# Performance work log

Hardware: AMD Instinct MI355X
Metric: run time of the kernel (lower is better)

The kernel has to match this reference:

```python
import jax, jax.numpy as jnp
import numpy as np

NUM_HEADS = 32  # head_dim = input_dim // num_heads = 32 == C (forced by matmul contraction)


def setup_inputs() -> dict:
    key = jax.random.key(0)
    ks = jax.random.split(key, 8)
    B, C, D3, H1 = 16, 32, 1, 32
    input_dim = 1024  # == C**2, forced by the final view(B, C, H1, W1)
    s = 0.02
    x1 = jax.random.normal(ks[0], (B, C, D3, H1, input_dim), jnp.float32)
    x2 = jax.random.normal(ks[1], (B, C, D3, H1, input_dim), jnp.float32)
    Wq = jax.random.normal(ks[2], (input_dim, input_dim), jnp.float32) * s
    bq = jax.random.normal(ks[3], (input_dim,), jnp.float32) * s
    Wk = jax.random.normal(ks[4], (input_dim, input_dim), jnp.float32) * s
    bk = jax.random.normal(ks[5], (input_dim,), jnp.float32) * s
    Wv = jax.random.normal(ks[6], (input_dim, input_dim), jnp.float32) * s
    bv = jax.random.normal(ks[7], (input_dim,), jnp.float32) * s
    return {"x1": x1, "x2": x2, "Wq": Wq, "bq": bq, "Wk": Wk, "bk": bk, "Wv": Wv, "bv": bv}


def reference(x1, x2, Wq, bq, Wk, bk, Wv, bv):
    B, C, _, H1, W1 = x1.shape  # W1 == input_dim (Linear acts on last dim)
    nh = NUM_HEADS
    hd = W1 // nh
    # Linear projections on the last axis (torch Linear: x @ W.T + b)
    q = (x1 @ Wq.T + bq).reshape(B, C, nh, hd, -1).transpose(0, 2, 4, 3, 1)  # (B, nh, L1, hd, C)
    k = (x2 @ Wk.T + bk).reshape(B, C, nh, hd, -1)                            # (B, C, nh, hd, L2)
    v = (x2 @ Wv.T + bv).reshape(B, C, nh, hd, -1)                            # (B, C, nh, hd, L2)
    # Broadcasted batched matmul: contracts q's trailing C axis with k's hd axis (C == hd).
    energy = jnp.matmul(q, k)                      # (B, C, L1, hd, L2)
    attention = jax.nn.softmax(energy, axis=-1)    # softmax over L2
    # Contracts v's L2 axis with attention's hd axis (L2 == hd).
    out = jnp.matmul(v, attention)                 # (B, C, L1, hd, L2)
    out = out.transpose(0, 2, 4, 3, 1).reshape(B, C, H1, W1)
    return out
```

## Files before the change

### kernel.cpp

```cpp
#include <hip/hip_runtime.h>
#include <cstdint>

typedef __bf16 bf16x8 __attribute__((ext_vector_type(8)));
typedef float f32x4 __attribute__((ext_vector_type(4)));
typedef unsigned short us8 __attribute__((ext_vector_type(8)));

__device__ __forceinline__ unsigned short f2bf(float f) {
  union { float f; uint32_t u; } c; c.f = f;
  uint32_t u = c.u + 0x7FFFu + ((c.u >> 16) & 1u);
  return (unsigned short)(u >> 16);
}

__global__ __launch_bounds__(256) void cvt5(
    const float* __restrict__ x1, const float* __restrict__ x2,
    const float* __restrict__ Wq, const float* __restrict__ Wk, const float* __restrict__ Wv,
    unsigned short* __restrict__ xb1, unsigned short* __restrict__ xb2,
    unsigned short* __restrict__ wb) {
  int z = blockIdx.y;
  const float* src; unsigned short* dst; int n4;
  if (z == 0)      { src = x1; dst = xb1;            n4 = 16777216 / 4; }
  else if (z == 1) { src = x2; dst = xb2;            n4 = 16777216 / 4; }
  else if (z == 2) { src = Wq; dst = wb;             n4 = 1048576 / 4; }
  else if (z == 3) { src = Wk; dst = wb + 1048576;   n4 = 1048576 / 4; }
  else             { src = Wv; dst = wb + 2*1048576; n4 = 1048576 / 4; }
  for (int i = blockIdx.x * 256 + threadIdx.x; i < n4; i += gridDim.x * 256) {
    float4 v = ((const float4*)src)[i];
    ushort4 o;
    o.x = f2bf(v.x); o.y = f2bf(v.y); o.z = f2bf(v.z); o.w = f2bf(v.w);
    ((ushort4*)dst)[i] = o;
  }
}

__global__ __launch_bounds__(256) void gemm_qkv(
    const unsigned short* __restrict__ xb1, const unsigned short* __restrict__ xb2,
    const unsigned short* __restrict__ wb,
    const float* __restrict__ bq, const float* __restrict__ bk, const float* __restrict__ bv,
    unsigned short* __restrict__ qkv) {
  __shared__ __attribute__((aligned(16))) unsigned short lA[128 * 32];
  __shared__ __attribute__((aligned(16))) unsigned short lB[128 * 32];
  const int id = blockIdx.x;
  const int xcd = id & 7;
  const int j = id >> 3;
  const int nb = j & 7;
  const int g = j >> 3;
  const int z = g >> 4;
  const int mb = (g & 15) * 8 + xcd;
  const unsigned short* A = (z == 0) ? xb1 : xb2;
  const unsigned short* W = wb + z * 1048576;
  const float* bias = (z == 0) ? bq : (z == 1 ? bk : bv);
  unsigned short* C = qkv + z * 16777216;
  const int n0 = nb * 128;
  const int m0 = mb * 128;
  const int lane = threadIdx.x & 63;
  const int wv = threadIdx.x >> 6;
  const int wm = wv >> 1, wn = wv & 1;
  const int mr = lane & 15, quad = lane >> 4;

  f32x4 acc[4][4];
#pragma unroll
  for (int i = 0; i < 4; ++i)
#pragma unroll
    for (int jj = 0; jj < 4; ++jj) acc[i][jj] = (f32x4){0.f, 0.f, 0.f, 0.f};

  for (int k0 = 0; k0 < 1024; k0 += 32) {
#pragma unroll
    for (int c4 = 0; c4 < 4; ++c4) {
      int c = wv * 4 + c4;
      int isB = c >> 3;
      int cc = c & 7;
      int row = cc * 16 + (lane >> 2);
      const unsigned short* src = isB ? (W + (n0 + row) * 1024 + k0)
                                      : (A + (m0 + row) * 1024 + k0);
      const char* gp = (const char*)src + (lane & 3) * 16;
      char* ldst = (char*)(isB ? lB : lA) + cc * 1024;
      __builtin_amdgcn_global_load_lds((const __attribute__((address_space(1))) void*)gp,
                                       (__attribute__((address_space(3))) void*)ldst,
                                       16, 0, 0);
    }
    __syncthreads();
    bf16x8 af[4], bfr[4];
#pragma unroll
    for (int i = 0; i < 4; ++i)
      af[i] = *(const bf16x8*)(lA + (wm * 64 + i * 16 + mr) * 32 + quad * 8);
#pragma unroll
    for (int jj = 0; jj < 4; ++jj)
      bfr[jj] = *(const bf16x8*)(lB + (wn * 64 + jj * 16 + mr) * 32 + quad * 8);
#pragma unroll
    for (int i = 0; i < 4; ++i)
#pragma unroll
      for (int jj = 0; jj < 4; ++jj)
        acc[i][jj] = __builtin_amdgcn_mfma_f32_16x16x32_bf16(af[i], bfr[jj], acc[i][jj], 0, 0, 0);
    __syncthreads();
  }
#pragma unroll
  for (int jj = 0; jj < 4; ++jj) {
    int col = n0 + wn * 64 + jj * 16 + mr;
    float bb = bias[col];
#pragma unroll
    for (int i = 0; i < 4; ++i) {
      int rbase = m0 + wm * 64 + i * 16 + quad * 4;
#pragma unroll
      for (int r = 0; r < 4; ++r)
        C[(rbase + r) * 1024 + col] = f2bf(acc[i][jj][r] + bb);
    }
  }
}

__global__ __launch_bounds__(256) void attn(const unsigned short* __restrict__ qkv,
                                            float* __restrict__ obuf) {
  const unsigned short* qbuf = qkv;
  const unsigned short* kbuf = qkv + 16777216;
  const unsigned short* vbuf = qkv + 2 * 16777216;
  __shared__ __attribute__((aligned(16))) unsigned short qs[8192];
  __shared__ __attribute__((aligned(16))) unsigned short ks[4][1024];
  __shared__ __attribute__((aligned(16))) unsigned short vs[4][1024];
  __shared__ __attribute__((aligned(16))) unsigned short ats[4][1024];
  const int id = blockIdx.x;
  const int xcd = id & 7;
  const int pos = id >> 3;
  const int y0 = (pos & 3) * 8;
  const int bx = (pos >> 2) * 8 + xcd;
  const int b = bx >> 5;
  const int x = bx & 31;
  const int lane = threadIdx.x & 63;
  const int wv = threadIdx.x >> 6;
  const int mr = lane & 15, quad = lane >> 4;

#pragma unroll
  for (int it = 0; it < 4; ++it) {
    int c = threadIdx.x + 256 * it;
    int t = c >> 5, m = c & 31;
    const uint4* src = (const uint4*)(qbuf + ((b * 1024 + t * 32 + x) * 1024 + m * 32 + y0));
    ((uint4*)qs)[c] = *src;
  }
  __syncthreads();

  for (int s = 0; s < 2; ++s) {
    int y = y0 + wv * 2 + s;
    int dy = wv * 2 + s;
    const unsigned short* krow = kbuf + ((b * 32 + x) * 32 + y) * 1024;
    const unsigned short* vrow = vbuf + ((b * 32 + x) * 32 + y) * 1024;
    ((uint4*)ks[wv])[lane] = ((const uint4*)krow)[lane];
    ((uint4*)ks[wv])[64 + lane] = ((const uint4*)krow)[64 + lane];
    ((uint4*)vs[wv])[lane] = ((const uint4*)vrow)[lane];
    ((uint4*)vs[wv])[64 + lane] = ((const uint4*)vrow)[64 + lane];

    bf16x8 qa[2], kb[2];
#pragma unroll
    for (int mt = 0; mt < 2; ++mt) {
      us8 tmp;
#pragma unroll
      for (int jj = 0; jj < 8; ++jj)
        tmp[jj] = qs[((quad * 8 + jj) * 32 + mt * 16 + mr) * 8 + dy];
      qa[mt] = __builtin_bit_cast(bf16x8, tmp);
    }
#pragma unroll
    for (int lt = 0; lt < 2; ++lt) {
      us8 tmp;
#pragma unroll
      for (int jj = 0; jj < 8; ++jj)
        tmp[jj] = ks[wv][(quad * 8 + jj) * 32 + lt * 16 + mr];
      kb[lt] = __builtin_bit_cast(bf16x8, tmp);
    }
    f32x4 e[2][2];
#pragma unroll
    for (int mt = 0; mt < 2; ++mt)
#pragma unroll
      for (int lt = 0; lt < 2; ++lt) {
        f32x4 zz = (f32x4){0.f, 0.f, 0.f, 0.f};
        e[mt][lt] = __builtin_amdgcn_mfma_f32_16x16x32_bf16(qa[mt], kb[lt], zz, 0, 0, 0);
      }

#pragma unroll
    for (int mt = 0; mt < 2; ++mt)
#pragma unroll
      for (int r = 0; r < 4; ++r) {
        float v0 = e[mt][0][r], v1 = e[mt][1][r];
        float mx = fmaxf(v0, v1);
#pragma unroll
        for (int off = 1; off < 16; off <<= 1) mx = fmaxf(mx, __shfl_xor(mx, off));
        float p0 = __expf(v0 - mx), p1 = __expf(v1 - mx);
        float sm = p0 + p1;
#pragma unroll
        for (int off = 1; off < 16; off <<= 1) sm += __shfl_xor(sm, off);
        float inv = 1.0f / sm;
        p0 *= inv; p1 *= inv;
        int trow = mt * 16 + quad * 4 + r;
        ats[wv][trow * 32 + mr] = f2bf(p0);
        ats[wv][trow * 32 + 16 + mr] = f2bf(p1);
      }

    bf16x8 va[2], pb[2];
#pragma unroll
    for (int i = 0; i < 2; ++i)
      va[i] = *(const bf16x8*)(&vs[wv][(i * 16 + mr) * 32 + quad * 8]);
#pragma unroll
    for (int lt = 0; lt < 2; ++lt) {
      us8 tmp;
#pragma unroll
      for (int jj = 0; jj < 8; ++jj)
        tmp[jj] = ats[wv][(quad * 8 + jj) * 32 + lt * 16 + mr];
      pb[lt] = __builtin_bit_cast(bf16x8, tmp);
    }
    f32x4 o[2][2];
#pragma unroll
    for (int i = 0; i < 2; ++i)
#pragma unroll
      for (int lt = 0; lt < 2; ++lt) {
        f32x4 zz = (f32x4){0.f, 0.f, 0.f, 0.f};
        o[i][lt] = __builtin_amdgcn_mfma_f32_16x16x32_bf16(va[i], pb[lt], zz, 0, 0, 0);
      }

    float* orow = obuf + ((b * 32 + x) * 32 + y) * 1024;
#pragma unroll
    for (int i = 0; i < 2; ++i)
#pragma unroll
      for (int lt = 0; lt < 2; ++lt)
#pragma unroll
        for (int r = 0; r < 4; ++r)
          orow[(i * 16 + quad * 4 + r) * 32 + lt * 16 + mr] = o[i][lt][r];
  }
}

__global__ __launch_bounds__(256) void transpose2(const float* __restrict__ obuf,
                                                  float* __restrict__ out) {
  __shared__ float t[2][32][33];
  const int y = blockIdx.y, b = blockIdx.z;
  int l = threadIdx.x & 31;
  int g = threadIdx.x >> 5;
#pragma unroll
  for (int mi = 0; mi < 8; ++mi) {
    int m = blockIdx.x * 8 + mi;
    int buf = mi & 1;
    for (int xx = g; xx < 32; xx += 8)
      t[buf][xx][l] = obuf[((b * 32 + xx) * 32 + y) * 1024 + m * 32 + l];
    __syncthreads();
    for (int ll = g; ll < 32; ll += 8)
      out[((b * 32 + y) * 32 + ll) * 1024 + m * 32 + l] = t[buf][l][ll];
  }
}

extern "C" void kernel_launch(void* const* d_in, const int* in_sizes, int n_in,
                              void* d_out, int out_size, void* d_ws, size_t ws_size,
                              hipStream_t stream) {
  const float* x1 = (const float*)d_in[0];
  const float* x2 = (const float*)d_in[1];
  const float* Wq = (const float*)d_in[2];
  const float* bq = (const float*)d_in[3];
  const float* Wk = (const float*)d_in[4];
  const float* bk = (const float*)d_in[5];
  const float* Wv = (const float*)d_in[6];
  const float* bv = (const float*)d_in[7];
  float* out = (float*)d_out;

  char* ws = (char*)d_ws;
  unsigned short* xb1 = (unsigned short*)ws;
  unsigned short* xb2 = xb1 + 16777216;
  unsigned short* wb = xb2 + 16777216;
  unsigned short* qkv = wb + 3 * 1048576;
  float* obuf = (float*)ws;

  cvt5<<<dim3(2048, 5), 256, 0, stream>>>(x1, x2, Wq, Wk, Wv, xb1, xb2, wb);
  gemm_qkv<<<dim3(3072), 256, 0, stream>>>(xb1, xb2, wb, bq, bk, bv, qkv);
  attn<<<dim3(2048), 256, 0, stream>>>(qkv, obuf);
  transpose2<<<dim3(4, 32, 16), 256, 0, stream>>>(obuf, out);
}
```

Measured before the change: 360.5 us.

## Rewrite QKV GEMM as 256x256 double-buffered pipelined kernel with swizzled LDS

Replaces the 128x128, single-buffered QKV projection GEMM with a 256x256 tile, 512-thread kernel using BK=64. Global-to-LDS loads are double-buffered and interleaved with MFMA phases under barriers and setprio. The LDS layout uses an XOR swizzle to avoid bank conflicts. Block IDs are remapped per XCD for cache locality. The aim is to hide load latency and raise data reuse in the dominant GEMM, at the cost of 128KB of LDS per block, lower occupancy and a fragile hand-written waitcnt schedule.

Result: no change. 357.6 us (-0.8%).

```diff
diff --git a/kernel.cpp b/kernel.cpp
--- a/kernel.cpp
+++ b/kernel.cpp
@@ -31,77 +31,161 @@
   }
 }
 
-__global__ __launch_bounds__(256) void gemm_qkv(
+__device__ __forceinline__ void stage_half(const unsigned short* __restrict__ g,
+                                           unsigned short* l, int wv, int rl, int cg) {
+#pragma unroll
+  for (int ld = 0; ld < 2; ++ld) {
+    const int chunk = wv * 2 + ld;
+    const unsigned short* gp = g + (chunk * 8 + rl) * 1024 + cg * 8;
+    unsigned short* lp = l + chunk * 512;
+    __builtin_amdgcn_global_load_lds((const __attribute__((address_space(1))) void*)gp,
+                                     (__attribute__((address_space(3))) void*)lp,
+                                     16, 0, 0);
+  }
+}
+
+__global__ __launch_bounds__(512) void gemm_qkv(
     const unsigned short* __restrict__ xb1, const unsigned short* __restrict__ xb2,
     const unsigned short* __restrict__ wb,
     const float* __restrict__ bq, const float* __restrict__ bk, const float* __restrict__ bv,
     unsigned short* __restrict__ qkv) {
-  __shared__ __attribute__((aligned(16))) unsigned short lA[128 * 32];
-  __shared__ __attribute__((aligned(16))) unsigned short lB[128 * 32];
+  __shared__ __attribute__((aligned(16))) unsigned short sm[65536];
+  unsigned short* lA0 = sm;
+  unsigned short* lB0 = sm + 16384;
+  unsigned short* lA1 = sm + 32768;
+  unsigned short* lB1 = sm + 49152;
+
   const int id = blockIdx.x;
-  const int xcd = id & 7;
-  const int j = id >> 3;
-  const int nb = j & 7;
-  const int g = j >> 3;
-  const int z = g >> 4;
-  const int mb = (g & 15) * 8 + xcd;
-  const unsigned short* A = (z == 0) ? xb1 : xb2;
-  const unsigned short* W = wb + z * 1048576;
+  const int swz = (id & 7) * 96 + (id >> 3);
+  const int z = swz >> 8;
+  const int rem = swz & 255;
+  const int mb = rem >> 2;
+  const int nb = rem & 3;
+  const int m0 = mb * 256;
+  const int n0 = nb * 256;
+
+  const unsigned short* Ag = (z == 0) ? xb1 : xb2;
+  const unsigned short* Wg = wb + z * 1048576;
   const float* bias = (z == 0) ? bq : (z == 1 ? bk : bv);
   unsigned short* C = qkv + z * 16777216;
-  const int n0 = nb * 128;
-  const int m0 = mb * 128;
-  const int lane = threadIdx.x & 63;
-  const int wv = threadIdx.x >> 6;
-  const int wm = wv >> 1, wn = wv & 1;
-  const int mr = lane & 15, quad = lane >> 4;
-
-  f32x4 acc[4][4];
-#pragma unroll
-  for (int i = 0; i < 4; ++i)
-#pragma unroll
-    for (int jj = 0; jj < 4; ++jj) acc[i][jj] = (f32x4){0.f, 0.f, 0.f, 0.f};
-
-  for (int k0 = 0; k0 < 1024; k0 += 32) {
-#pragma unroll
-    for (int c4 = 0; c4 < 4; ++c4) {
-      int c = wv * 4 + c4;
-      int isB = c >> 3;
-      int cc = c & 7;
-      int row = cc * 16 + (lane >> 2);
-      const unsigned short* src = isB ? (W + (n0 + row) * 1024 + k0)
-                                      : (A + (m0 + row) * 1024 + k0);
-      const char* gp = (const char*)src + (lane & 3) * 16;
-      char* ldst = (char*)(isB ? lB : lA) + cc * 1024;
-      __builtin_amdgcn_global_load_lds((const __attribute__((address_space(1))) void*)gp,
-                                       (__attribute__((address_space(3))) void*)ldst,
-                                       16, 0, 0);
-    }
-    __syncthreads();
-    bf16x8 af[4], bfr[4];
+
+  const int tid = threadIdx.x;
+  const int lane = tid & 63;
+  const int wv = tid >> 6;
+  const int wm = wv >> 2;
+  const int wn = wv & 3;
+  const int mr = lane & 15;
+  const int quad = lane >> 4;
+
+  const int rl = lane >> 3;
+  const int cg = (lane & 7) ^ rl;
+
+  const int sg0 = ((quad) ^ (mr & 7)) * 8;
+  const int sg1 = ((4 + quad) ^ (mr & 7)) * 8;
+  const int arow = (wm * 128 + mr) * 64;
+  const int brow = (wn * 64 + mr) * 64;
+
+  f32x4 acc[8][4];
+#pragma unroll
+  for (int i = 0; i < 8; ++i)
+#pragma unroll
+    for (int j = 0; j < 4; ++j) acc[i][j] = (f32x4){0.f, 0.f, 0.f, 0.f};
+
+  bf16x8 af[4][2], bfr[4][2];
+
+  auto STA = [&](unsigned short* dst, int kt) {
+    const unsigned short* g = Ag + m0 * 1024 + kt * 64;
+    stage_half(g, dst, wv, rl, cg);
+    stage_half(g + 128 * 1024, dst + 8192, wv, rl, cg);
+  };
+  auto STB = [&](unsigned short* dst, int kt) {
+    const unsigned short* g = Wg + n0 * 1024 + kt * 64;
+    stage_half(g, dst, wv, rl, cg);
+    stage_half(g + 128 * 1024, dst + 8192, wv, rl, cg);
+  };
+  auto RDA = [&](const unsigned short* lA, int ib) {
+#pragma unroll
+    for (int i = 0; i < 4; ++i) {
+      af[i][0] = *(const bf16x8*)(lA + arow + (ib + i) * 1024 + sg0);
+      af[i][1] = *(const bf16x8*)(lA + arow + (ib + i) * 1024 + sg1);
+    }
+  };
+  auto RDB = [&](const unsigned short* lB, int jb) {
+#pragma unroll
+    for (int j = 0; j < 2; ++j) {
+      bfr[jb + j][0] = *(const bf16x8*)(lB + brow + (jb + j) * 1024 + sg0);
+      bfr[jb + j][1] = *(const bf16x8*)(lB + brow + (jb + j) * 1024 + sg1);
+    }
+  };
+  auto MF = [&](int ib, int jb) {
 #pragma unroll
     for (int i = 0; i < 4; ++i)
-      af[i] = *(const bf16x8*)(lA + (wm * 64 + i * 16 + mr) * 32 + quad * 8);
-#pragma unroll
-    for (int jj = 0; jj < 4; ++jj)
-      bfr[jj] = *(const bf16x8*)(lB + (wn * 64 + jj * 16 + mr) * 32 + quad * 8);
-#pragma unroll
-    for (int i = 0; i < 4; ++i)
-#pragma unroll
-      for (int jj = 0; jj < 4; ++jj)
-        acc[i][jj] = __builtin_amdgcn_mfma_f32_16x16x32_bf16(af[i], bfr[jj], acc[i][jj], 0, 0, 0);
-    __syncthreads();
-  }
-#pragma unroll
-  for (int jj = 0; jj < 4; ++jj) {
-    int col = n0 + wn * 64 + jj * 16 + mr;
-    float bb = bias[col];
-#pragma unroll
-    for (int i = 0; i < 4; ++i) {
-      int rbase = m0 + wm * 64 + i * 16 + quad * 4;
+#pragma unroll
+      for (int j = 0; j < 2; ++j)
+#pragma unroll
+        for (int h = 0; h < 2; ++h)
+          acc[ib + i][jb + j] = __builtin_amdgcn_mfma_f32_16x16x32_bf16(
+              af[i][h], bfr[jb + j][h], acc[ib + i][jb + j], 0, 0, 0);
+  };
+
+  STA(lA0, 0);
+  STB(lB0, 0);
+  STA(lA1, 1);
+  asm volatile("s_waitcnt vmcnt(4)" ::: "memory");
+  __builtin_amdgcn_s_barrier();
+
+#pragma unroll 1
+  for (int t = 0; t < 8; ++t) {
+    const bool lastt = (t == 7);
+    RDA(lA0, 0); RDB(lB0, 0);
+    STB(lB1, 2 * t + 1);
+    __builtin_amdgcn_s_barrier();
+    __builtin_amdgcn_s_setprio(1); MF(0, 0); __builtin_amdgcn_s_setprio(0);
+    __builtin_amdgcn_s_barrier();
+    RDB(lB0, 2);
+    __builtin_amdgcn_s_barrier();
+    __builtin_amdgcn_s_setprio(1); MF(0, 2); __builtin_amdgcn_s_setprio(0);
+    __builtin_amdgcn_s_barrier();
+    RDA(lA0, 4);
+    __builtin_amdgcn_s_barrier();
+    __builtin_amdgcn_s_setprio(1); MF(4, 0); __builtin_amdgcn_s_setprio(0);
+    __builtin_amdgcn_s_barrier();
+    if (!lastt) STA(lA0, 2 * t + 2);
+    __builtin_amdgcn_s_barrier();
+    __builtin_amdgcn_s_setprio(1); MF(4, 2); __builtin_amdgcn_s_setprio(0);
+    if (lastt) { asm volatile("s_waitcnt vmcnt(0)" ::: "memory"); }
+    else       { asm volatile("s_waitcnt vmcnt(4)" ::: "memory"); }
+    __builtin_amdgcn_s_barrier();
+    RDA(lA1, 0); RDB(lB1, 0);
+    if (!lastt) STB(lB0, 2 * t + 2);
+    __builtin_amdgcn_s_barrier();
+    __builtin_amdgcn_s_setprio(1); MF(0, 0); __builtin_amdgcn_s_setprio(0);
+    __builtin_amdgcn_s_barrier();
+    RDB(lB1, 2);
+    __builtin_amdgcn_s_barrier();
+    __builtin_amdgcn_s_setprio(1); MF(0, 2); __builtin_amdgcn_s_setprio(0);
+    __builtin_amdgcn_s_barrier();
+    RDA(lA1, 4);
+    __builtin_amdgcn_s_barrier();
+    __builtin_amdgcn_s_setprio(1); MF(4, 0); __builtin_amdgcn_s_setprio(0);
+    __builtin_amdgcn_s_barrier();
+    if (!lastt) STA(lA1, 2 * t + 3);
+    __builtin_amdgcn_s_barrier();
+    __builtin_amdgcn_s_setprio(1); MF(4, 2); __builtin_amdgcn_s_setprio(0);
+    if (!lastt) { asm volatile("s_waitcnt vmcnt(4)" ::: "memory"); }
+    __builtin_amdgcn_s_barrier();
+  }
+
+#pragma unroll
+  for (int j = 0; j < 4; ++j) {
+    const int col = n0 + wn * 64 + j * 16 + mr;
+    const float bb = bias[col];
+#pragma unroll
+    for (int i = 0; i < 8; ++i) {
+      const int rb = m0 + wm * 128 + i * 16 + quad * 4;
 #pragma unroll
       for (int r = 0; r < 4; ++r)
-        C[(rbase + r) * 1024 + col] = f2bf(acc[i][jj][r] + bb);
+        C[(rb + r) * 1024 + col] = f2bf(acc[i][j][r] + bb);
     }
   }
 }
@@ -261,7 +345,7 @@
   float* obuf = (float*)ws;
 
   cvt5<<<dim3(2048, 5), 256, 0, stream>>>(x1, x2, Wq, Wk, Wv, xb1, xb2, wb);
-  gemm_qkv<<<dim3(3072), 256, 0, stream>>>(xb1, xb2, wb, bq, bk, bv, qkv);
+  gemm_qkv<<<dim3(768), 512, 0, stream>>>(xb1, xb2, wb, bq, bk, bv, qkv);
   attn<<<dim3(2048), 256, 0, stream>>>(qkv, obuf);
   transpose2<<<dim3(4, 32, 16), 256, 0, stream>>>(obuf, out);
 }
```
